# Kernel optimization log

Measured on AMD Instinct MI355X. Metric: run time of the kernel, lower is better.

## Reference

```python
import jax, jax.numpy as jnp
import numpy as np

N, C, L = 64, 3, 4096
K, S = 128, 64  # num_shapelets, shapelets_size


def setup_inputs() -> dict:
    key = jax.random.key(0)
    kx, ks = jax.random.split(key)
    x = jax.random.normal(kx, (N, C, L), dtype=jnp.float32)
    shapelets = jax.random.normal(ks, (C, K, S), dtype=jnp.float32)
    return {"x": x, "shapelets": shapelets}


def _min_euclid(x, shapelets):
    # x: (N, C, L); shapelets: (C, K, S)
    # Torch does unfold -> cdist -> min over windows -> min over channels.
    # We compute ||x_w - s||^2 = ||x_w||^2 + ||s||^2 - 2<x_w, s> with sliding
    # dot products via grouped 1-D conv (avoids materializing the unfold).
    C_, K_, S_ = shapelets.shape
    n = x.shape[0]
    filt = shapelets.reshape(C_ * K_, 1, S_)  # OIW, grouped by channel
    dots = jax.lax.conv_general_dilated(
        x, filt, window_strides=(1,), padding="VALID",
        dimension_numbers=("NCW", "OIW", "NCW"),
        feature_group_count=C_)                      # (N, C*K, W)
    ones = jnp.ones((C_, 1, S_), x.dtype)
    x2 = jax.lax.conv_general_dilated(
        x * x, ones, window_strides=(1,), padding="VALID",
        dimension_numbers=("NCW", "OIW", "NCW"),
        feature_group_count=C_)                      # (N, C, W) sliding ||x_w||^2
    W_ = dots.shape[-1]
    dots = dots.reshape(n, C_, K_, W_)               # (N, C, K, W)
    s2 = jnp.sum(shapelets * shapelets, axis=-1)     # (C, K)
    d2 = x2[:, :, None, :] + s2[None, :, :, None] - 2.0 * dots
    d = jnp.sqrt(jnp.maximum(d2, 0.0))               # Euclidean distance (N,C,K,W)
    d = jnp.min(d, axis=3)                           # min over windows -> (N, C, K)
    d = jnp.min(d, axis=1)                           # min over channels -> (N, K)
    return d[:, None, :]                             # (N, 1, K)


def reference(x, shapelets):
    return _min_euclid(x, shapelets)
```

## Files before the change

### kernel.cpp

```cpp
#include <hip/hip_runtime.h>

#define NN 64
#define CC 3
#define LL 4096
#define SS 64
#define KK 128
#define WW 4033
#define BLKN 8

typedef __attribute__((ext_vector_type(8))) short v8s;
typedef __attribute__((ext_vector_type(4))) float v4f;

#define WS_CNT_OFF 32768
#define WS_HS2_OFF 33024
#define WS_SHB_OFF 34560

__device__ __forceinline__ unsigned bf16_rne(float f) {
    unsigned u = __float_as_uint(f);
    return (u + 0x7FFFu + ((u >> 16) & 1u)) >> 16;
}

__global__ __launch_bounds__(256) void me_prep(
        const float* __restrict__ shp,
        unsigned* __restrict__ d2g,
        unsigned* __restrict__ cnt,
        float* __restrict__ hs2g,
        uint4* __restrict__ shb) {
    const int tid = blockIdx.x * 256 + threadIdx.x;
    d2g[tid] = 0x7F800000u;
    if (tid < NN) cnt[tid] = 0u;
    if (tid < CC * KK) {
        const float4* r4 = (const float4*)(shp + (size_t)tid * SS);
        float a = 0.f;
        #pragma unroll
        for (int i = 0; i < 16; ++i) {
            float4 v = r4[i];
            a += v.x * v.x + v.y * v.y + v.z * v.z + v.w * v.w;
        }
        hs2g[tid] = -0.5f * a;
    }
    if (tid < CC * 1024) {
        int c   = tid >> 10;
        int r   = tid & 1023;
        int nt  = r >> 7;
        int scb = (r >> 6) & 1;
        int l   = r & 63;
        int row  = nt * 16 + (l & 15);
        int koff = scb * 32 + (l >> 4) * 8;
        const float* s = shp + ((size_t)(c * KK + row)) * SS + koff;
        float4 f0 = *(const float4*)s;
        float4 f1 = *(const float4*)(s + 4);
        uint4 o;
        o.x = (bf16_rne(f0.y) << 16) | bf16_rne(f0.x);
        o.y = (bf16_rne(f0.w) << 16) | bf16_rne(f0.z);
        o.z = (bf16_rne(f1.y) << 16) | bf16_rne(f1.x);
        o.w = (bf16_rne(f1.w) << 16) | bf16_rne(f1.z);
        shb[tid] = o;
    }
}

__global__ __launch_bounds__(256, 2) void me_main(
        const float* __restrict__ x,
        const ushort* __restrict__ shb_g,
        const float* __restrict__ hs2g,
        unsigned* __restrict__ d2g,
        unsigned* __restrict__ cnt,
        float* __restrict__ out) {

    __shared__ __align__(16) ushort shb[CC * 8192];
    __shared__ __align__(8) ushort xs2[2][2][CC][320];
    __shared__ __align__(16) float Ps[CC][320];
    __shared__ __align__(16) float hx[CC][256];
    __shared__ unsigned red[KK];
    __shared__ int lastflag;

    const int b    = blockIdx.x;
    const int n    = b >> 3;
    const int tg   = b & 7;
    const int t    = threadIdx.x;
    const int lane = t & 63, wave = t >> 6;
    const int quad = lane >> 4, col = lane & 15;
    const int wbase = wave * 64;

    if (t < KK) red[t] = 0x7F800000u;

    {
        typedef __attribute__((address_space(1))) const uint4 gu4;
        typedef __attribute__((address_space(3))) uint4 lu4;
        const uint4* gbase = (const uint4*)shb_g;
        #pragma unroll
        for (int it = 0; it < 12; ++it) {
            const uint4* gp = gbase + it * 256 + t;
            uint4* lp = (uint4*)shb + (it * 256 + wave * 64);
            __builtin_amdgcn_global_load_lds((gu4*)gp, (lu4*)lp, 16, 0, 0);
        }
    }

    float hsv[CC][8];
    #pragma unroll
    for (int c = 0; c < CC; ++c)
        #pragma unroll
        for (int nt = 0; nt < 8; ++nt)
            hsv[c][nt] = hs2g[c * KK + nt * 16 + col];

    const float* xb = x + (size_t)n * (CC * LL);

    float rmax[8];
    #pragma unroll
    for (int nt = 0; nt < 8; ++nt) rmax[nt] = -3.4e38f;

    for (int it = 0; it < 2; ++it) {
        const int buf = it;
        const int w0  = tg * 512 + it * 256;

        if (t < 240) {
            int c = t / 80, q = t - c * 80;
            int idx = q * 4, gi = w0 + idx;
            float4 v;
            if (gi + 3 < LL) v = *(const float4*)(xb + c * LL + gi);
            else {
                v.x = (gi     < LL) ? xb[c * LL + gi]     : 0.f;
                v.y = (gi + 1 < LL) ? xb[c * LL + gi + 1] : 0.f;
                v.z = (gi + 2 < LL) ? xb[c * LL + gi + 2] : 0.f;
                v.w = (gi + 3 < LL) ? xb[c * LL + gi + 3] : 0.f;
            }
            unsigned h0 = bf16_rne(v.x), h1 = bf16_rne(v.y);
            unsigned h2 = bf16_rne(v.z), h3 = bf16_rne(v.w);
            uint2 p0; p0.x = h0 | (h1 << 16); p0.y = h2 | (h3 << 16);
            *(uint2*)&xs2[buf][0][c][idx] = p0;
            if (idx > 0) xs2[buf][1][c][idx - 1] = (ushort)h0;
            *(uint*)&xs2[buf][1][c][idx] = h1 | (h2 << 16);
            xs2[buf][1][c][idx + 2] = (ushort)h3;
        }
        if (wave < CC) {
            const float* xp = xb + wave * LL + w0;
            float qq[5];
            #pragma unroll
            for (int i = 0; i < 5; ++i) {
                int idx = lane * 5 + i;
                float v = (w0 + idx < LL) ? xp[idx] : 0.f;
                qq[i] = v * v;
            }
            float run = 0.f;
            #pragma unroll
            for (int i = 0; i < 5; ++i) { run += qq[i]; qq[i] = run; }
            float sc = run;
            #pragma unroll
            for (int d = 1; d < 64; d <<= 1) {
                float u = __shfl_up(sc, d, 64);
                if (lane >= d) sc += u;
            }
            float excl = sc - run;
            #pragma unroll
            for (int i = 0; i < 5; ++i) Ps[wave][lane * 5 + i] = qq[i] + excl;
        }
        __syncthreads();

        {
            int w = t;
            #pragma unroll
            for (int c = 0; c < CC; ++c) {
                float I1 = Ps[c][w + 63];
                float I0 = (w > 0) ? Ps[c][w - 1] : 0.f;
                float o = -0.5f * (I1 - I0);
                if (w0 + w >= WW) o = -1e30f;
                hx[c][w] = o;
            }
        }
        __syncthreads();

        #pragma unroll
        for (int c = 0; c < CC; ++c) {
            v4f hxv[4];
            #pragma unroll
            for (int mt = 0; mt < 4; ++mt)
                hxv[mt] = *(const v4f*)&hx[c][wbase + mt * 16 + quad * 4];
            v8s af[4][2];
            #pragma unroll
            for (int mt = 0; mt < 4; ++mt)
                #pragma unroll
                for (int sc = 0; sc < 2; ++sc) {
                    int e0 = wbase + mt * 16 + col + sc * 32 + quad * 8;
                    int p  = col & 1;
                    const uint* ap = (const uint*)&xs2[buf][p][c][e0 - p];
                    union { v8s v; uint u[4]; } au;
                    au.u[0] = ap[0]; au.u[1] = ap[1];
                    au.u[2] = ap[2]; au.u[3] = ap[3];
                    af[mt][sc] = au.v;
                }
            #pragma unroll
            for (int g = 0; g < 2; ++g) {
                v4f acc[4][4];
                #pragma unroll
                for (int nt2 = 0; nt2 < 4; ++nt2) {
                    float h = hsv[c][g * 4 + nt2];
                    v4f a = {h, h, h, h};
                    #pragma unroll
                    for (int mt = 0; mt < 4; ++mt) acc[nt2][mt] = a;
                }
                #pragma unroll
                for (int sc = 0; sc < 2; ++sc)
                    #pragma unroll
                    for (int nt2 = 0; nt2 < 4; ++nt2) {
                        int nt = g * 4 + nt2;
                        v8s bfr = *(const v8s*)(shb + (((c * 8 + nt) * 2 + sc) * 64 + lane) * 8);
                        #pragma unroll
                        for (int mt = 0; mt < 4; ++mt)
                            acc[nt2][mt] = __builtin_amdgcn_mfma_f32_16x16x32_bf16(
                                af[mt][sc], bfr, acc[nt2][mt], 0, 0, 0);
                    }
                #pragma unroll
                for (int nt2 = 0; nt2 < 4; ++nt2) {
                    float m = -3.4e38f;
                    #pragma unroll
                    for (int mt = 0; mt < 4; ++mt) {
                        v4f a = acc[nt2][mt];
                        #pragma unroll
                        for (int r = 0; r < 4; ++r)
                            m = fmaxf(m, a[r] + hxv[mt][r]);
                    }
                    rmax[g * 4 + nt2] = fmaxf(rmax[g * 4 + nt2], m);
                }
            }
        }
    }

    #pragma unroll
    for (int nt = 0; nt < 8; ++nt) {
        float v = rmax[nt];
        v = fmaxf(v, __shfl_xor(v, 16, 64));
        v = fmaxf(v, __shfl_xor(v, 32, 64));
        rmax[nt] = v;
    }
    if (quad == 0) {
        #pragma unroll
        for (int nt = 0; nt < 8; ++nt) {
            float d2 = fmaxf(-2.f * rmax[nt], 0.f);
            atomicMin(&red[nt * 16 + col], __float_as_uint(d2));
        }
    }
    __syncthreads();
    if (t < KK) atomicMin(&d2g[n * KK + t], red[t]);

    __syncthreads();
    if (t == 0) {
        unsigned old = atomicAdd(&cnt[n], 1u);
        lastflag = (old == BLKN - 1) ? 1 : 0;
    }
    __syncthreads();
    if (lastflag && t < KK) {
        unsigned bits = atomicMin(&d2g[n * KK + t], 0x7F800000u);
        out[n * KK + t] = sqrtf(__uint_as_float(bits));
    }
}

extern "C" void kernel_launch(void* const* d_in, const int* in_sizes, int n_in,
                              void* d_out, int out_size, void* d_ws, size_t ws_size,
                              hipStream_t stream) {
    const float* x   = (const float*)d_in[0];
    const float* shp = (const float*)d_in[1];
    unsigned* d2g  = (unsigned*)d_ws;
    unsigned* cnt  = (unsigned*)((char*)d_ws + WS_CNT_OFF);
    float*    hs2g = (float*)((char*)d_ws + WS_HS2_OFF);
    uint4*    shb  = (uint4*)((char*)d_ws + WS_SHB_OFF);
    float* out = (float*)d_out;

    hipLaunchKernelGGL(me_prep, dim3(32), dim3(256), 0, stream,
                       shp, d2g, cnt, hs2g, shb);
    hipLaunchKernelGGL(me_main, dim3(NN * BLKN), dim3(256), 0, stream,
                       x, (const ushort*)shb, hs2g, d2g, cnt, out);
}
```

Measured before the change: 74.45 us.

## Software-pipeline x tile staging with MFMA compute and compute prefix-sum windows in registers

Splits the per-iteration staging into a load phase and a store phase so the second tile's global loads are issued before computing the first tile, overlapping memory latency with MFMA work. The windowed squared-norm is now formed from the wave-level prefix sum with shuffles directly in registers, which removes the Ps shared buffer and one barrier per iteration. hx is double-buffered to allow this overlap. It also adds thread fences around the completion counter, which adds a little cost but makes the cross-block reduction ordering safer.

```diff
diff --git a/kernel.cpp b/kernel.cpp
--- a/kernel.cpp
+++ b/kernel.cpp
@@ -69,8 +69,7 @@
 
     __shared__ __align__(16) ushort shb[CC * 8192];
     __shared__ __align__(8) ushort xs2[2][2][CC][320];
-    __shared__ __align__(16) float Ps[CC][320];
-    __shared__ __align__(16) float hx[CC][256];
+    __shared__ __align__(16) float hx[2][CC][256];
     __shared__ unsigned red[KK];
     __shared__ int lastflag;
 
@@ -105,84 +104,104 @@
 
     const float* xb = x + (size_t)n * (CC * LL);
 
+    const bool do_stage = (t < 240);
+    const int  cs   = t / 80;
+    const int  sidx = (t - cs * 80) * 4;
+
+    float4 stv;
+    float  qq[5];
+
+    auto load_xt = [&](int it) {
+        const int w0 = tg * 512 + it * 256;
+        if (do_stage) {
+            int gi = w0 + sidx;
+            const float* xc = xb + cs * LL;
+            if (gi + 3 < LL) stv = *(const float4*)(xc + gi);
+            else {
+                stv.x = (gi     < LL) ? xc[gi]     : 0.f;
+                stv.y = (gi + 1 < LL) ? xc[gi + 1] : 0.f;
+                stv.z = (gi + 2 < LL) ? xc[gi + 2] : 0.f;
+                stv.w = (gi + 3 < LL) ? xc[gi + 3] : 0.f;
+            }
+        }
+        if (wave < CC) {
+            const float* xp = xb + wave * LL + w0;
+            #pragma unroll
+            for (int i = 0; i < 5; ++i) {
+                int idx = lane * 5 + i;
+                qq[i] = (w0 + idx < LL) ? xp[idx] : 0.f;
+            }
+        }
+    };
+
+    auto store_xt = [&](int it) {
+        const int w0 = tg * 512 + it * 256;
+        if (do_stage) {
+            unsigned h0 = bf16_rne(stv.x), h1 = bf16_rne(stv.y);
+            unsigned h2 = bf16_rne(stv.z), h3 = bf16_rne(stv.w);
+            uint2 p0; p0.x = h0 | (h1 << 16); p0.y = h2 | (h3 << 16);
+            *(uint2*)&xs2[it][0][cs][sidx] = p0;
+            if (sidx > 0) xs2[it][1][cs][sidx - 1] = (ushort)h0;
+            *(uint*)&xs2[it][1][cs][sidx] = h1 | (h2 << 16);
+            xs2[it][1][cs][sidx + 2] = (ushort)h3;
+        }
+        if (wave < CC) {
+            float p[5]; float runv = 0.f;
+            #pragma unroll
+            for (int i = 0; i < 5; ++i) { runv += qq[i] * qq[i]; p[i] = runv; }
+            float scv = runv;
+            #pragma unroll
+            for (int d = 1; d < 64; d <<= 1) {
+                float u = __shfl_up(scv, d, 64);
+                if (lane >= d) scv += u;
+            }
+            float excl = scv - runv;
+            #pragma unroll
+            for (int i = 0; i < 5; ++i) p[i] += excl;
+            float hi0 = __shfl_down(p[3], 12, 64);
+            float hi1 = __shfl_down(p[4], 12, 64);
+            float hi2 = __shfl_down(p[0], 13, 64);
+            float hi3 = __shfl_down(p[1], 13, 64);
+            float hi4 = __shfl_down(p[2], 13, 64);
+            float up4 = __shfl_up(p[4], 1, 64);
+            float hi[5] = {hi0, hi1, hi2, hi3, hi4};
+            float lo[5];
+            lo[0] = (lane == 0) ? 0.f : up4;
+            lo[1] = p[0]; lo[2] = p[1]; lo[3] = p[2]; lo[4] = p[3];
+            int wb = lane * 5;
+            if (wb < 256) {
+                #pragma unroll
+                for (int i = 0; i < 5; ++i) {
+                    int w = wb + i;
+                    if (w < 256) {
+                        float o = -0.5f * (hi[i] - lo[i]);
+                        if (w0 + w >= WW) o = -1e30f;
+                        hx[it][wave][w] = o;
+                    }
+                }
+            }
+        }
+    };
+
     float rmax[8];
     #pragma unroll
     for (int nt = 0; nt < 8; ++nt) rmax[nt] = -3.4e38f;
 
-    for (int it = 0; it < 2; ++it) {
-        const int buf = it;
-        const int w0  = tg * 512 + it * 256;
-
-        if (t < 240) {
-            int c = t / 80, q = t - c * 80;
-            int idx = q * 4, gi = w0 + idx;
-            float4 v;
-            if (gi + 3 < LL) v = *(const float4*)(xb + c * LL + gi);
-            else {
-                v.x = (gi     < LL) ? xb[c * LL + gi]     : 0.f;
-                v.y = (gi + 1 < LL) ? xb[c * LL + gi + 1] : 0.f;
-                v.z = (gi + 2 < LL) ? xb[c * LL + gi + 2] : 0.f;
-                v.w = (gi + 3 < LL) ? xb[c * LL + gi + 3] : 0.f;
-            }
-            unsigned h0 = bf16_rne(v.x), h1 = bf16_rne(v.y);
-            unsigned h2 = bf16_rne(v.z), h3 = bf16_rne(v.w);
-            uint2 p0; p0.x = h0 | (h1 << 16); p0.y = h2 | (h3 << 16);
-            *(uint2*)&xs2[buf][0][c][idx] = p0;
-            if (idx > 0) xs2[buf][1][c][idx - 1] = (ushort)h0;
-            *(uint*)&xs2[buf][1][c][idx] = h1 | (h2 << 16);
-            xs2[buf][1][c][idx + 2] = (ushort)h3;
-        }
-        if (wave < CC) {
-            const float* xp = xb + wave * LL + w0;
-            float qq[5];
-            #pragma unroll
-            for (int i = 0; i < 5; ++i) {
-                int idx = lane * 5 + i;
-                float v = (w0 + idx < LL) ? xp[idx] : 0.f;
-                qq[i] = v * v;
-            }
-            float run = 0.f;
-            #pragma unroll
-            for (int i = 0; i < 5; ++i) { run += qq[i]; qq[i] = run; }
-            float sc = run;
-            #pragma unroll
-            for (int d = 1; d < 64; d <<= 1) {
-                float u = __shfl_up(sc, d, 64);
-                if (lane >= d) sc += u;
-            }
-            float excl = sc - run;
-            #pragma unroll
-            for (int i = 0; i < 5; ++i) Ps[wave][lane * 5 + i] = qq[i] + excl;
-        }
-        __syncthreads();
-
-        {
-            int w = t;
-            #pragma unroll
-            for (int c = 0; c < CC; ++c) {
-                float I1 = Ps[c][w + 63];
-                float I0 = (w > 0) ? Ps[c][w - 1] : 0.f;
-                float o = -0.5f * (I1 - I0);
-                if (w0 + w >= WW) o = -1e30f;
-                hx[c][w] = o;
-            }
-        }
-        __syncthreads();
-
+    auto compute = [&](int it) {
         #pragma unroll
         for (int c = 0; c < CC; ++c) {
             v4f hxv[4];
             #pragma unroll
             for (int mt = 0; mt < 4; ++mt)
-                hxv[mt] = *(const v4f*)&hx[c][wbase + mt * 16 + quad * 4];
+                hxv[mt] = *(const v4f*)&hx[it][c][wbase + mt * 16 + quad * 4];
             v8s af[4][2];
             #pragma unroll
             for (int mt = 0; mt < 4; ++mt)
                 #pragma unroll
                 for (int sc = 0; sc < 2; ++sc) {
                     int e0 = wbase + mt * 16 + col + sc * 32 + quad * 8;
-                    int p  = col & 1;
-                    const uint* ap = (const uint*)&xs2[buf][p][c][e0 - p];
+                    int pp = col & 1;
+                    const uint* ap = (const uint*)&xs2[it][pp][c][e0 - pp];
                     union { v8s v; uint u[4]; } au;
                     au.u[0] = ap[0]; au.u[1] = ap[1];
                     au.u[2] = ap[2]; au.u[3] = ap[3];
@@ -223,7 +242,16 @@
                 }
             }
         }
-    }
+    };
+
+    load_xt(0);
+    store_xt(0);
+    __syncthreads();
+    load_xt(1);
+    compute(0);
+    store_xt(1);
+    __syncthreads();
+    compute(1);
 
     #pragma unroll
     for (int nt = 0; nt < 8; ++nt) {
@@ -241,13 +269,14 @@
     }
     __syncthreads();
     if (t < KK) atomicMin(&d2g[n * KK + t], red[t]);
-
+    __threadfence();
     __syncthreads();
     if (t == 0) {
         unsigned old = atomicAdd(&cnt[n], 1u);
         lastflag = (old == BLKN - 1) ? 1 : 0;
     }
     __syncthreads();
+    __threadfence();
     if (lastflag && t < KK) {
         unsigned bits = atomicMin(&d2g[n * KK + t], 0x7F800000u);
         out[n * KK + t] = sqrtf(__uint_as_float(bits));
```

Measured after the change: 200.2 us. +169.0%, slower.

## Software-pipeline x staging with MFMA compute and scan prefix sums in registers

Applied to the files above, without the earlier changes.

Unrolls the two-iteration loop so the global loads for the second tile are issued before the first tile's MFMA compute, overlapping memory latency with math. The prefix-sum window energy is now formed with wave shuffles instead of a shared-memory Ps buffer, which removes one barrier per tile. The hx term is folded into the accumulator initialisation rather than added in the max epilogue, and A fragments are deduplicated from 8 to 6 LDS loads. The trade-off is more live registers under the 2-blocks-per-SM launch bound, plus the shuffle index logic must be correct.

```diff
diff --git a/kernel.cpp b/kernel.cpp
--- a/kernel.cpp
+++ b/kernel.cpp
@@ -59,6 +59,137 @@
     }
 }
 
+
+#define LOADX(W0, SV, QQ) do {                                               \
+    if (do_stage) {                                                          \
+        int gi = (W0) + sidx;                                                \
+        const float* xcs = xb + cs * LL;                                     \
+        if (gi + 3 < LL) SV = *(const float4*)(xcs + gi);                    \
+        else {                                                               \
+            SV.x = (gi     < LL) ? xcs[gi]     : 0.f;                        \
+            SV.y = (gi + 1 < LL) ? xcs[gi + 1] : 0.f;                        \
+            SV.z = (gi + 2 < LL) ? xcs[gi + 2] : 0.f;                        \
+            SV.w = (gi + 3 < LL) ? xcs[gi + 3] : 0.f;                        \
+        }                                                                    \
+    }                                                                        \
+    if (do_scan) {                                                           \
+        const float* xp = xb + wave * LL + (W0);                             \
+        _Pragma("unroll")                                                    \
+        for (int i = 0; i < 5; ++i) {                                        \
+            int idx = lane * 5 + i;                                          \
+            QQ[i] = ((W0) + idx < LL) ? xp[idx] : 0.f;                       \
+        }                                                                    \
+    } } while (0)
+
+#define STAGE_STORE(BUF, SV) do {                                            \
+    if (do_stage) {                                                          \
+        unsigned h0 = bf16_rne(SV.x), h1 = bf16_rne(SV.y);                   \
+        unsigned h2 = bf16_rne(SV.z), h3 = bf16_rne(SV.w);                   \
+        uint2 p0; p0.x = h0 | (h1 << 16); p0.y = h2 | (h3 << 16);            \
+        *(uint2*)&xs2[BUF][0][cs][sidx] = p0;                    \
+        if (sidx > 0) xs2[BUF][1][cs][sidx - 1] = (ushort)h0;    \
+        *(uint*)&xs2[BUF][1][cs][sidx] = h1 | (h2 << 16);                    \
+        xs2[BUF][1][cs][sidx + 2] = (ushort)h3;                              \
+    } } while (0)
+
+#define SCANHX(BUF, W0, QQ) do {                                             \
+    if (do_scan) {                                                           \
+        float p[5]; float runv = 0.f;                                        \
+        _Pragma("unroll")                                                    \
+        for (int i = 0; i < 5; ++i) { runv += QQ[i] * QQ[i]; p[i] = runv; }  \
+        float scv = runv;                                                    \
+        _Pragma("unroll")                                                    \
+        for (int d = 1; d < 64; d <<= 1) {                                   \
+            float u = __shfl_up(scv, d, 64);                                 \
+            if (lane >= d) scv += u;                                         \
+        }                                                                    \
+        float excl = scv - runv;                                             \
+        _Pragma("unroll")                                                    \
+        for (int i = 0; i < 5; ++i) p[i] += excl;                            \
+                            \
+        float hi_[5];                                                        \
+        hi_[0] = __shfl_down(p[3], 12, 64);                                  \
+        hi_[1] = __shfl_down(p[4], 12, 64);                                  \
+        hi_[2] = __shfl_down(p[0], 13, 64);                                  \
+        hi_[3] = __shfl_down(p[1], 13, 64);                                  \
+        hi_[4] = __shfl_down(p[2], 13, 64);                                  \
+        float up4 = __shfl_up(p[4], 1, 64);                                  \
+        float lo_[5];                                                        \
+        lo_[0] = (lane == 0) ? 0.f : up4;                                    \
+        lo_[1] = p[0]; lo_[2] = p[1]; lo_[3] = p[2]; lo_[4] = p[3];          \
+        int wb = lane * 5;                                                   \
+        if (wb < 256) {                                     \
+            _Pragma("unroll")                                                \
+            for (int i = 0; i < 5; ++i) {                                    \
+                int w = wb + i;                                              \
+                if (w < 256) {                                               \
+                    float o = -0.5f * (hi_[i] - lo_[i]);                     \
+                    if ((W0) + w >= WW) o = -1e30f;          \
+                    hx[BUF][wave][w] = o;                                    \
+                }                                                            \
+            }                                                                \
+        }                                                                    \
+    } } while (0)
+
+#define COMPUTE(BUF) do {                                                    \
+    _Pragma("unroll")                                                        \
+    for (int c = 0; c < CC; ++c) {                                           \
+        v4f hxv[4];                                                          \
+        _Pragma("unroll")                                                    \
+        for (int mt = 0; mt < 4; ++mt)                                       \
+            hxv[mt] = *(const v4f*)&hx[BUF][c][wbase + mt * 16 + quad * 4];  \
+             \
+        v8s afu[6];                                                          \
+        _Pragma("unroll")                                                    \
+        for (int u = 0; u < 6; ++u) {                                        \
+            int e0 = wbase + u * 16 + col + quad * 8;                        \
+            int pp = col & 1;                                                \
+            const uint* ap = (const uint*)&xs2[BUF][pp][c][e0 - pp];         \
+            union { v8s v; uint w4[4]; } au;                                 \
+            au.w4[0] = ap[0]; au.w4[1] = ap[1];                              \
+            au.w4[2] = ap[2]; au.w4[3] = ap[3];                              \
+            afu[u] = au.v;                                                   \
+        }                                                                    \
+        _Pragma("unroll")                                                    \
+        for (int g = 0; g < 2; ++g) {                                        \
+            v4f acc[4][4];         \
+            _Pragma("unroll")                                                \
+            for (int nt2 = 0; nt2 < 4; ++nt2) {                              \
+                float h = hsv[c][g * 4 + nt2];                               \
+                _Pragma("unroll")                                            \
+                for (int mt = 0; mt < 4; ++mt) {                             \
+                    v4f a = hxv[mt];                                         \
+                    a[0] += h; a[1] += h; a[2] += h; a[3] += h;              \
+                    acc[nt2][mt] = a;                                        \
+                }                                                            \
+            }                                                                \
+            _Pragma("unroll")                                                \
+            for (int sc = 0; sc < 2; ++sc)                                   \
+                _Pragma("unroll")                                            \
+                for (int nt2 = 0; nt2 < 4; ++nt2) {                          \
+                    int nt = g * 4 + nt2;                                    \
+                    v8s bfr = *(const v8s*)(shb +                            \
+                        (((c * 8 + nt) * 2 + sc) * 64 + lane) * 8);          \
+                    _Pragma("unroll")                                        \
+                    for (int mt = 0; mt < 4; ++mt)                           \
+                        acc[nt2][mt] = __builtin_amdgcn_mfma_f32_16x16x32_bf16( \
+                            afu[mt + 2 * sc], bfr, acc[nt2][mt], 0, 0, 0);   \
+                }                                                            \
+                            \
+            _Pragma("unroll")                                                \
+            for (int nt2 = 0; nt2 < 4; ++nt2) {                              \
+                float m = -3.4e38f;                                          \
+                _Pragma("unroll")                                            \
+                for (int mt = 0; mt < 4; ++mt) {                             \
+                    v4f a = acc[nt2][mt];                                    \
+                    _Pragma("unroll")                                        \
+                    for (int r = 0; r < 4; ++r) m = fmaxf(m, a[r]);          \
+                }                                                            \
+                rmax[g * 4 + nt2] = fmaxf(rmax[g * 4 + nt2], m);             \
+            }                                                                \
+        }                                                                    \
+    } } while (0)
+
 __global__ __launch_bounds__(256, 2) void me_main(
         const float* __restrict__ x,
         const ushort* __restrict__ shb_g,
@@ -69,8 +200,7 @@
 
     __shared__ __align__(16) ushort shb[CC * 8192];
     __shared__ __align__(8) ushort xs2[2][2][CC][320];
-    __shared__ __align__(16) float Ps[CC][320];
-    __shared__ __align__(16) float hx[CC][256];
+    __shared__ __align__(16) float hx[2][CC][256];
     __shared__ unsigned red[KK];
     __shared__ int lastflag;
 
@@ -105,125 +235,31 @@
 
     const float* xb = x + (size_t)n * (CC * LL);
 
+    const bool do_stage = (t < 240);
+    const int  cs   = t / 80;
+    const int  sidx = (t - cs * 80) * 4;
+    const bool do_scan = (wave < CC);
+
     float rmax[8];
     #pragma unroll
     for (int nt = 0; nt < 8; ++nt) rmax[nt] = -3.4e38f;
 
-    for (int it = 0; it < 2; ++it) {
-        const int buf = it;
-        const int w0  = tg * 512 + it * 256;
-
-        if (t < 240) {
-            int c = t / 80, q = t - c * 80;
-            int idx = q * 4, gi = w0 + idx;
-            float4 v;
-            if (gi + 3 < LL) v = *(const float4*)(xb + c * LL + gi);
-            else {
-                v.x = (gi     < LL) ? xb[c * LL + gi]     : 0.f;
-                v.y = (gi + 1 < LL) ? xb[c * LL + gi + 1] : 0.f;
-                v.z = (gi + 2 < LL) ? xb[c * LL + gi + 2] : 0.f;
-                v.w = (gi + 3 < LL) ? xb[c * LL + gi + 3] : 0.f;
-            }
-            unsigned h0 = bf16_rne(v.x), h1 = bf16_rne(v.y);
-            unsigned h2 = bf16_rne(v.z), h3 = bf16_rne(v.w);
-            uint2 p0; p0.x = h0 | (h1 << 16); p0.y = h2 | (h3 << 16);
-            *(uint2*)&xs2[buf][0][c][idx] = p0;
-            if (idx > 0) xs2[buf][1][c][idx - 1] = (ushort)h0;
-            *(uint*)&xs2[buf][1][c][idx] = h1 | (h2 << 16);
-            xs2[buf][1][c][idx + 2] = (ushort)h3;
-        }
-        if (wave < CC) {
-            const float* xp = xb + wave * LL + w0;
-            float qq[5];
-            #pragma unroll
-            for (int i = 0; i < 5; ++i) {
-                int idx = lane * 5 + i;
-                float v = (w0 + idx < LL) ? xp[idx] : 0.f;
-                qq[i] = v * v;
-            }
-            float run = 0.f;
-            #pragma unroll
-            for (int i = 0; i < 5; ++i) { run += qq[i]; qq[i] = run; }
-            float sc = run;
-            #pragma unroll
-            for (int d = 1; d < 64; d <<= 1) {
-                float u = __shfl_up(sc, d, 64);
-                if (lane >= d) sc += u;
-            }
-            float excl = sc - run;
-            #pragma unroll
-            for (int i = 0; i < 5; ++i) Ps[wave][lane * 5 + i] = qq[i] + excl;
-        }
-        __syncthreads();
-
-        {
-            int w = t;
-            #pragma unroll
-            for (int c = 0; c < CC; ++c) {
-                float I1 = Ps[c][w + 63];
-                float I0 = (w > 0) ? Ps[c][w - 1] : 0.f;
-                float o = -0.5f * (I1 - I0);
-                if (w0 + w >= WW) o = -1e30f;
-                hx[c][w] = o;
-            }
-        }
-        __syncthreads();
-
-        #pragma unroll
-        for (int c = 0; c < CC; ++c) {
-            v4f hxv[4];
-            #pragma unroll
-            for (int mt = 0; mt < 4; ++mt)
-                hxv[mt] = *(const v4f*)&hx[c][wbase + mt * 16 + quad * 4];
-            v8s af[4][2];
-            #pragma unroll
-            for (int mt = 0; mt < 4; ++mt)
-                #pragma unroll
-                for (int sc = 0; sc < 2; ++sc) {
-                    int e0 = wbase + mt * 16 + col + sc * 32 + quad * 8;
-                    int p  = col & 1;
-                    const uint* ap = (const uint*)&xs2[buf][p][c][e0 - p];
-                    union { v8s v; uint u[4]; } au;
-                    au.u[0] = ap[0]; au.u[1] = ap[1];
-                    au.u[2] = ap[2]; au.u[3] = ap[3];
-                    af[mt][sc] = au.v;
-                }
-            #pragma unroll
-            for (int g = 0; g < 2; ++g) {
-                v4f acc[4][4];
-                #pragma unroll
-                for (int nt2 = 0; nt2 < 4; ++nt2) {
-                    float h = hsv[c][g * 4 + nt2];
-                    v4f a = {h, h, h, h};
-                    #pragma unroll
-                    for (int mt = 0; mt < 4; ++mt) acc[nt2][mt] = a;
-                }
-                #pragma unroll
-                for (int sc = 0; sc < 2; ++sc)
-                    #pragma unroll
-                    for (int nt2 = 0; nt2 < 4; ++nt2) {
-                        int nt = g * 4 + nt2;
-                        v8s bfr = *(const v8s*)(shb + (((c * 8 + nt) * 2 + sc) * 64 + lane) * 8);
-                        #pragma unroll
-                        for (int mt = 0; mt < 4; ++mt)
-                            acc[nt2][mt] = __builtin_amdgcn_mfma_f32_16x16x32_bf16(
-                                af[mt][sc], bfr, acc[nt2][mt], 0, 0, 0);
-                    }
-                #pragma unroll
-                for (int nt2 = 0; nt2 < 4; ++nt2) {
-                    float m = -3.4e38f;
-                    #pragma unroll
-                    for (int mt = 0; mt < 4; ++mt) {
-                        v4f a = acc[nt2][mt];
-                        #pragma unroll
-                        for (int r = 0; r < 4; ++r)
-                            m = fmaxf(m, a[r] + hxv[mt][r]);
-                    }
-                    rmax[g * 4 + nt2] = fmaxf(rmax[g * 4 + nt2], m);
-                }
-            }
-        }
-    }
+    const int w0a = tg * 512;
+    const int w0b = tg * 512 + 256;
+
+    float4 sv0; float q0[5];
+    LOADX(w0a, sv0, q0);
+    STAGE_STORE(0, sv0);
+    SCANHX(0, w0a, q0);
+    __syncthreads();
+
+    float4 sv1; float q1[5];
+    LOADX(w0b, sv1, q1);
+    COMPUTE(0);
+    STAGE_STORE(1, sv1);
+    SCANHX(1, w0b, q1);
+    __syncthreads();
+    COMPUTE(1);
 
     #pragma unroll
     for (int nt = 0; nt < 8; ++nt) {
```

Measured after the change: 107.6 us. 1.45x slower.
